# Kernel optimization log

Measured on AMD Instinct MI355X. Metric: run time of the kernel, lower is better.

Reference implementation:

```python
import jax, jax.numpy as jnp
import numpy as np

IN_D = 4096
OUT_D = 4096
NNZ = 1677722
BATCH = 4096
NEG_SLOPE = 0.1


def setup_inputs() -> dict:
    key = jax.random.key(0)
    k_x, k_w, k_b, k_r, k_c = jax.random.split(key, 5)
    x = jax.random.normal(k_x, (BATCH, IN_D), dtype=jnp.float32)
    weight = jax.random.normal(k_w, (NNZ,), dtype=jnp.float32)
    bias = jax.random.normal(k_b, (OUT_D,), dtype=jnp.float32)
    rows = jax.random.randint(k_r, (NNZ,), 0, IN_D, dtype=jnp.int32)
    cols = jax.random.randint(k_c, (NNZ,), 0, OUT_D, dtype=jnp.int32)
    return {"x": x, "weight": weight, "bias": bias, "rows": rows, "cols": cols}


def reference(x, weight, bias, rows, cols):
    # Sparse.forward: W = zeros(in_d, out_d); W[loc] = weight; rho(bias + x @ W)
    W = jnp.zeros((IN_D, OUT_D), dtype=x.dtype).at[rows, cols].set(weight)
    return jax.nn.leaky_relu(bias + x @ W, negative_slope=NEG_SLOPE)
```

## Files before the change

### kernel.cpp

```cpp
#include <hip/hip_runtime.h>
#include <stdint.h>

#define IN_D  4096
#define OUT_D 4096
#define BATCH 4096
#define NEG_SLOPE 0.1f
#define NSEG 8
#define SEGCAP 192

typedef __attribute__((ext_vector_type(8))) short short8;
typedef __attribute__((ext_vector_type(4))) float f32x4;

__device__ __forceinline__ unsigned short f2bf(float f) {
    unsigned u = __builtin_bit_cast(unsigned, f);
    u += 0x7FFFu + ((u >> 16) & 1u);
    return (unsigned short)(u >> 16);
}

__device__ __forceinline__ void gload_lds16(const unsigned short* gsrc, unsigned short* ldsp) {
    __builtin_amdgcn_global_load_lds(
        (const __attribute__((address_space(1))) unsigned int*)gsrc,
        (__attribute__((address_space(3))) unsigned int*)ldsp,
        16, 0, 0);
}

__global__ void zerocnt_kernel(uint4* __restrict__ cnt4) {
    int i = blockIdx.x * blockDim.x + threadIdx.x;
    cnt4[i] = make_uint4(0u, 0u, 0u, 0u);
}

__global__ void bucketcvt_kernel(const int* __restrict__ rows, const int* __restrict__ cols,
                                 const float* __restrict__ w,
                                 unsigned* __restrict__ cnt, uint2* __restrict__ bucket,
                                 int nnz,
                                 const float4* __restrict__ x, ushort4* __restrict__ xb,
                                 int nx4) {
    const int stride = gridDim.x * blockDim.x;
    const int i0 = blockIdx.x * blockDim.x + threadIdx.x;
    const int g = blockIdx.x & (NSEG - 1);
    for (int i = i0; i < nnz; i += stride) {
        int c = cols[i];
        unsigned pos = atomicAdd(&cnt[g * OUT_D + c], 1u);
        if (pos < SEGCAP)
            bucket[((size_t)g * OUT_D + c) * SEGCAP + pos] =
                make_uint2((unsigned)rows[i] | ((unsigned)f2bf(w[i]) << 16),
                           (unsigned)(i + 1));
    }
    for (int i = i0; i < nx4; i += stride) {
        float4 v = x[i];
        ushort4 o;
        o.x = f2bf(v.x); o.y = f2bf(v.y); o.z = f2bf(v.z); o.w = f2bf(v.w);
        xb[i] = o;
    }
}

__global__ __launch_bounds__(256) void coldedup_kernel(
        const uint2* __restrict__ bucket, const unsigned* __restrict__ cnt,
        unsigned short* __restrict__ Wt) {
    __shared__ unsigned long long tag[IN_D];
    const int col = blockIdx.x;
    const int tid = threadIdx.x;

    uint4* t4 = (uint4*)tag;
    #pragma unroll
    for (int j = 0; j < 8; ++j) t4[tid + j * 256] = make_uint4(0u, 0u, 0u, 0u);
    __syncthreads();

    #pragma unroll
    for (int g = 0; g < NSEG; ++g) {
        const int n = min((int)cnt[g * OUT_D + col], SEGCAP);
        const uint2* bk = bucket + ((size_t)g * OUT_D + col) * SEGCAP;
        for (int e = tid; e < n; e += 256) {
            uint2 u = bk[e];
            unsigned long long v = ((unsigned long long)u.y << 16) | (u.x >> 16);
            atomicMax(&tag[u.x & 0xFFFu], v);
        }
    }
    __syncthreads();

    const int r0 = tid * 16;
    short8 o0, o1;
    #pragma unroll
    for (int j = 0; j < 8; ++j) {
        o0[j] = (short)(unsigned short)(tag[r0 + j] & 0xFFFFu);
        o1[j] = (short)(unsigned short)(tag[r0 + 8 + j] & 0xFFFFu);
    }
    *(short8*)&Wt[(size_t)col * IN_D + r0]     = o0;
    *(short8*)&Wt[(size_t)col * IN_D + r0 + 8] = o1;
}

#define BM 256
#define BN 256
#define BK 64
#define NT (IN_D / BK)

#define QUAD(MI0, NI0, BREG) \
    _Pragma("unroll") \
    for (int mi = 0; mi < 4; ++mi) { \
      _Pragma("unroll") \
      for (int ni = 0; ni < 2; ++ni) { \
        _Pragma("unroll") \
        for (int ks = 0; ks < 2; ++ks) { \
          acc[(MI0)+mi][(NI0)+ni] = __builtin_amdgcn_mfma_f32_16x16x32_bf16( \
              a[mi][ks], BREG[ni][ks], acc[(MI0)+mi][(NI0)+ni], 0, 0, 0); \
        } } }

#define PHASE_TAIL(QUADCALL) \
    __builtin_amdgcn_s_barrier(); \
    asm volatile("s_waitcnt lgkmcnt(0)" ::: "memory"); \
    __builtin_amdgcn_sched_barrier(0); \
    __builtin_amdgcn_s_setprio(1); \
    QUADCALL; \
    __builtin_amdgcn_s_setprio(0); \
    __builtin_amdgcn_s_barrier();

#define PREFETCH(D) \
    _Pragma("unroll") \
    for (int mi = 0; mi < 4; ++mi) { \
        a[mi][0] = *(const short8*)&lds[D][0][0][(jA_base + mi * 16) * 64 + kp0]; \
        a[mi][1] = *(const short8*)&lds[D][0][0][(jA_base + mi * 16) * 64 + kp1]; \
    } \
    b0[0][0] = *(const short8*)&lds[D][1][0][jB[0] * 64 + kp0]; \
    b0[0][1] = *(const short8*)&lds[D][1][0][jB[0] * 64 + kp1]; \
    b0[1][0] = *(const short8*)&lds[D][1][0][jB[1] * 64 + kp0]; \
    b0[1][1] = *(const short8*)&lds[D][1][0][jB[1] * 64 + kp1];

__global__ __launch_bounds__(512) void gemm_kernel(
        const unsigned short* __restrict__ Xb,
        const unsigned short* __restrict__ Wt,
        const float* __restrict__ bias,
        float* __restrict__ out)
{
    __shared__ unsigned short lds[2][2][2][128 * 64];

    const int tid  = threadIdx.x;
    const int lane = tid & 63;
    const int wave = tid >> 6;

    const int lin = blockIdx.y * 16 + blockIdx.x;
    const int swz = (lin & 7) * 32 + (lin >> 3);
    const int m0 = (swz >> 4) * BM;
    const int n0 = (swz & 15) * BN;

    const int wm = (wave >> 2) * 128;
    const int wn = (wave & 3) * 64;

    const int lr = lane & 15;
    const int kg = lane >> 4;
    const int x7 = lr & 7;
    const int l8 = lane >> 3;
    const int c8 = lane & 7;

    const int kp0 = ((0 * 4 + kg) ^ x7) * 8;
    const int kp1 = ((1 * 4 + kg) ^ x7) * 8;

    const int jA_base = (wave >> 2) * 64 + lr;
    int jB[4];
    #pragma unroll
    for (int ni = 0; ni < 4; ++ni) {
        int r16 = wn + ni * 16;
        jB[ni] = (r16 & 31) + ((r16 >> 6) << 5) + lr;
    }

    auto stageA = [&](int d, int h, int kt) {
        #pragma unroll
        for (int s = 0; s < 2; ++s) {
            int j = wave * 16 + s * 8 + l8;
            int trow = (j & 63) + h * 64 + ((j >> 6) << 7);
            const unsigned short* src =
                Xb + (size_t)(m0 + trow) * IN_D + kt * BK + 8 * (c8 ^ l8);
            gload_lds16(src, &lds[d][0][h][(wave * 16 + s * 8) * 64]);
        }
    };
    auto stageB = [&](int d, int h, int kt) {
        #pragma unroll
        for (int s = 0; s < 2; ++s) {
            int j = wave * 16 + s * 8 + l8;
            int trow = (j & 31) + h * 32 + ((j >> 5) << 6);
            const unsigned short* src =
                Wt + (size_t)(n0 + trow) * IN_D + kt * BK + 8 * (c8 ^ l8);
            gload_lds16(src, &lds[d][1][h][(wave * 16 + s * 8) * 64]);
        }
    };

    f32x4 acc[8][4] = {};
    short8 a[4][2], b0[2][2], b1[2][2];

    stageA(0, 0, 0); stageB(0, 0, 0); stageB(0, 1, 0); stageA(0, 1, 0);
    stageA(1, 0, 1); stageB(1, 1, 1); stageA(1, 1, 1); stageB(1, 0, 1);
    asm volatile("s_waitcnt vmcnt(8)" ::: "memory");
    __builtin_amdgcn_s_barrier();
    PREFETCH(0)
    asm volatile("s_waitcnt lgkmcnt(0)" ::: "memory");
    __builtin_amdgcn_sched_barrier(0);
    __builtin_amdgcn_s_setprio(1);
    QUAD(0, 0, b0)
    __builtin_amdgcn_s_setprio(0);
    __builtin_amdgcn_s_barrier();

    for (int t = 0; t < NT - 1; ++t) {
        const int cur = t & 1, nxt = cur ^ 1;
        const int kt2 = (t + 2) & (NT - 1);

        b1[0][0] = *(const short8*)&lds[cur][1][1][jB[2] * 64 + kp0];
        b1[0][1] = *(const short8*)&lds[cur][1][1][jB[2] * 64 + kp1];
        b1[1][0] = *(const short8*)&lds[cur][1][1][jB[3] * 64 + kp0];
        b1[1][1] = *(const short8*)&lds[cur][1][1][jB[3] * 64 + kp1];
        stageA(cur, 0, kt2);
        PHASE_TAIL(QUAD(0, 2, b1))

        #pragma unroll
        for (int mi = 0; mi < 4; ++mi) {
            a[mi][0] = *(const short8*)&lds[cur][0][1][(jA_base + mi * 16) * 64 + kp0];
            a[mi][1] = *(const short8*)&lds[cur][0][1][(jA_base + mi * 16) * 64 + kp1];
        }
        stageB(cur, 1, kt2);
        PHASE_TAIL(QUAD(4, 2, b1))

        stageA(cur, 1, kt2);
        asm volatile("s_waitcnt vmcnt(6)" ::: "memory");
        __builtin_amdgcn_s_barrier();
        asm volatile("s_waitcnt lgkmcnt(0)" ::: "memory");
        __builtin_amdgcn_sched_barrier(0);
        __builtin_amdgcn_s_setprio(1);
        QUAD(4, 0, b0)
        __builtin_amdgcn_s_setprio(0);
        PREFETCH(nxt)
        stageB(cur, 0, kt2);
        asm volatile("s_waitcnt lgkmcnt(0)" ::: "memory");
        __builtin_amdgcn_sched_barrier(0);
        __builtin_amdgcn_s_setprio(1);
        QUAD(0, 0, b0)
        __builtin_amdgcn_s_setprio(0);
        __builtin_amdgcn_s_barrier();
    }

    {
        const int cur = (NT - 1) & 1;
        b1[0][0] = *(const short8*)&lds[cur][1][1][jB[2] * 64 + kp0];
        b1[0][1] = *(const short8*)&lds[cur][1][1][jB[2] * 64 + kp1];
        b1[1][0] = *(const short8*)&lds[cur][1][1][jB[3] * 64 + kp0];
        b1[1][1] = *(const short8*)&lds[cur][1][1][jB[3] * 64 + kp1];
        PHASE_TAIL(QUAD(0, 2, b1))
        #pragma unroll
        for (int mi = 0; mi < 4; ++mi) {
            a[mi][0] = *(const short8*)&lds[cur][0][1][(jA_base + mi * 16) * 64 + kp0];
            a[mi][1] = *(const short8*)&lds[cur][0][1][(jA_base + mi * 16) * 64 + kp1];
        }
        asm volatile("s_waitcnt lgkmcnt(0)" ::: "memory");
        __builtin_amdgcn_sched_barrier(0);
        __builtin_amdgcn_s_setprio(1);
        QUAD(4, 2, b1)
        QUAD(4, 0, b0)
        __builtin_amdgcn_s_setprio(0);
    }

    float bfrag[4];
    #pragma unroll
    for (int ni = 0; ni < 4; ++ni) bfrag[ni] = bias[n0 + wn + ni * 16 + lr];

    #pragma unroll
    for (int mi = 0; mi < 8; ++mi) {
        #pragma unroll
        for (int ni = 0; ni < 4; ++ni) {
            const int col = n0 + wn + ni * 16 + lr;
            #pragma unroll
            for (int r = 0; r < 4; ++r) {
                const int row = m0 + wm + mi * 16 + kg * 4 + r;
                float v = acc[mi][ni][r] + bfrag[ni];
                v = v > 0.0f ? v : v * NEG_SLOPE;
                out[(size_t)row * OUT_D + col] = v;
            }
        }
    }
}

extern "C" void kernel_launch(void* const* d_in, const int* in_sizes, int n_in,
                              void* d_out, int out_size, void* d_ws, size_t ws_size,
                              hipStream_t stream) {
    const float* x    = (const float*)d_in[0];
    const float* w    = (const float*)d_in[1];
    const float* bias = (const float*)d_in[2];
    const int*   rows = (const int*)d_in[3];
    const int*   cols = (const int*)d_in[4];
    const int nnz = in_sizes[1];
    float* out = (float*)d_out;

    const size_t NW = (size_t)IN_D * OUT_D;
    unsigned*        cnt    = (unsigned*)d_ws;
    uint2*           bucket = (uint2*)((char*)d_ws + (1u << 20));
    unsigned short*  Wt     = (unsigned short*)((char*)d_ws + (1u << 20)
                                  + (size_t)NSEG * OUT_D * SEGCAP * 8);
    unsigned short*  Xb     = (unsigned short*)((char*)Wt + NW * 2);

    zerocnt_kernel<<<32, 256, 0, stream>>>((uint4*)cnt);
    bucketcvt_kernel<<<2048, 256, 0, stream>>>(rows, cols, w, cnt, bucket, nnz,
                                               (const float4*)x, (ushort4*)Xb,
                                               (int)((size_t)BATCH * IN_D / 4));
    coldedup_kernel<<<OUT_D, 256, 0, stream>>>(bucket, cnt, Wt);

    dim3 grid(OUT_D / BN, BATCH / BM);
    gemm_kernel<<<grid, 512, 0, stream>>>(Xb, Wt, bias, out);
}
```

Before: 204.8 us.

## Restructure GEMM main loop into two barrier phases and widen bucket segments

The GEMM k-loop drops from four compute phases per tile to two. The first half-tile of A/B fragments, including b1, is prefetched at the end of each iteration, and the global-to-LDS staging is regrouped to cut the barriers per iteration. Separately, the bucket scatter grows from 8 to 16 segments with a smaller per-segment capacity, and the counter-zeroing grid doubles to match, aiming to reduce atomic contention when building the dense weight. The new schedule changes vmcnt waits and LDS reuse timing, which risks overwriting buffers still being read or exposing more load latency. The smaller segment capacity may overflow on denser columns.

```diff
diff --git a/kernel.cpp b/kernel.cpp
--- a/kernel.cpp
+++ b/kernel.cpp
@@ -5,8 +5,8 @@
 #define OUT_D 4096
 #define BATCH 4096
 #define NEG_SLOPE 0.1f
-#define NSEG 8
-#define SEGCAP 192
+#define NSEG 16
+#define SEGCAP 120
 
 typedef __attribute__((ext_vector_type(8))) short short8;
 typedef __attribute__((ext_vector_type(4))) float f32x4;
@@ -105,16 +105,7 @@
               a[mi][ks], BREG[ni][ks], acc[(MI0)+mi][(NI0)+ni], 0, 0, 0); \
         } } }
 
-#define PHASE_TAIL(QUADCALL) \
-    __builtin_amdgcn_s_barrier(); \
-    asm volatile("s_waitcnt lgkmcnt(0)" ::: "memory"); \
-    __builtin_amdgcn_sched_barrier(0); \
-    __builtin_amdgcn_s_setprio(1); \
-    QUADCALL; \
-    __builtin_amdgcn_s_setprio(0); \
-    __builtin_amdgcn_s_barrier();
-
-#define PREFETCH(D) \
+#define PREFETCH3(D) \
     _Pragma("unroll") \
     for (int mi = 0; mi < 4; ++mi) { \
         a[mi][0] = *(const short8*)&lds[D][0][0][(jA_base + mi * 16) * 64 + kp0]; \
@@ -123,7 +114,11 @@
     b0[0][0] = *(const short8*)&lds[D][1][0][jB[0] * 64 + kp0]; \
     b0[0][1] = *(const short8*)&lds[D][1][0][jB[0] * 64 + kp1]; \
     b0[1][0] = *(const short8*)&lds[D][1][0][jB[1] * 64 + kp0]; \
-    b0[1][1] = *(const short8*)&lds[D][1][0][jB[1] * 64 + kp1];
+    b0[1][1] = *(const short8*)&lds[D][1][0][jB[1] * 64 + kp1]; \
+    b1[0][0] = *(const short8*)&lds[D][1][1][jB[2] * 64 + kp0]; \
+    b1[0][1] = *(const short8*)&lds[D][1][1][jB[2] * 64 + kp1]; \
+    b1[1][0] = *(const short8*)&lds[D][1][1][jB[3] * 64 + kp0]; \
+    b1[1][1] = *(const short8*)&lds[D][1][1][jB[3] * 64 + kp1];
 
 __global__ __launch_bounds__(512) void gemm_kernel(
         const unsigned short* __restrict__ Xb,
@@ -187,61 +182,53 @@
     short8 a[4][2], b0[2][2], b1[2][2];
 
     stageA(0, 0, 0); stageB(0, 0, 0); stageB(0, 1, 0); stageA(0, 1, 0);
-    stageA(1, 0, 1); stageB(1, 1, 1); stageA(1, 1, 1); stageB(1, 0, 1);
+    stageA(1, 0, 1); stageB(1, 0, 1); stageB(1, 1, 1); stageA(1, 1, 1);
     asm volatile("s_waitcnt vmcnt(8)" ::: "memory");
     __builtin_amdgcn_s_barrier();
-    PREFETCH(0)
-    asm volatile("s_waitcnt lgkmcnt(0)" ::: "memory");
-    __builtin_amdgcn_sched_barrier(0);
-    __builtin_amdgcn_s_setprio(1);
-    QUAD(0, 0, b0)
-    __builtin_amdgcn_s_setprio(0);
-    __builtin_amdgcn_s_barrier();
+    PREFETCH3(0)
 
     for (int t = 0; t < NT - 1; ++t) {
         const int cur = t & 1, nxt = cur ^ 1;
         const int kt2 = (t + 2) & (NT - 1);
 
-        b1[0][0] = *(const short8*)&lds[cur][1][1][jB[2] * 64 + kp0];
-        b1[0][1] = *(const short8*)&lds[cur][1][1][jB[2] * 64 + kp1];
-        b1[1][0] = *(const short8*)&lds[cur][1][1][jB[3] * 64 + kp0];
-        b1[1][1] = *(const short8*)&lds[cur][1][1][jB[3] * 64 + kp1];
+        asm volatile("s_waitcnt lgkmcnt(0)" ::: "memory");
+        __builtin_amdgcn_sched_barrier(0);
+        __builtin_amdgcn_s_setprio(1);
+        QUAD(0, 0, b0)
+        QUAD(0, 2, b1)
+        __builtin_amdgcn_s_setprio(0);
+        __builtin_amdgcn_s_barrier();
+
         stageA(cur, 0, kt2);
-        PHASE_TAIL(QUAD(0, 2, b1))
-
+        stageB(cur, 1, kt2);
+        stageB(cur, 0, kt2);
         #pragma unroll
         for (int mi = 0; mi < 4; ++mi) {
             a[mi][0] = *(const short8*)&lds[cur][0][1][(jA_base + mi * 16) * 64 + kp0];
             a[mi][1] = *(const short8*)&lds[cur][0][1][(jA_base + mi * 16) * 64 + kp1];
         }
-        stageB(cur, 1, kt2);
-        PHASE_TAIL(QUAD(4, 2, b1))
+        asm volatile("s_waitcnt lgkmcnt(0)" ::: "memory");
+        __builtin_amdgcn_sched_barrier(0);
+        __builtin_amdgcn_s_barrier();
 
         stageA(cur, 1, kt2);
-        asm volatile("s_waitcnt vmcnt(6)" ::: "memory");
+        __builtin_amdgcn_s_setprio(1);
+        QUAD(4, 2, b1)
+        QUAD(4, 0, b0)
+        __builtin_amdgcn_s_setprio(0);
+        asm volatile("s_waitcnt vmcnt(8)" ::: "memory");
         __builtin_amdgcn_s_barrier();
-        asm volatile("s_waitcnt lgkmcnt(0)" ::: "memory");
-        __builtin_amdgcn_sched_barrier(0);
-        __builtin_amdgcn_s_setprio(1);
-        QUAD(4, 0, b0)
-        __builtin_amdgcn_s_setprio(0);
-        PREFETCH(nxt)
-        stageB(cur, 0, kt2);
-        asm volatile("s_waitcnt lgkmcnt(0)" ::: "memory");
-        __builtin_amdgcn_sched_barrier(0);
-        __builtin_amdgcn_s_setprio(1);
-        QUAD(0, 0, b0)
-        __builtin_amdgcn_s_setprio(0);
-        __builtin_amdgcn_s_barrier();
+        PREFETCH3(nxt)
     }
 
     {
         const int cur = (NT - 1) & 1;
-        b1[0][0] = *(const short8*)&lds[cur][1][1][jB[2] * 64 + kp0];
-        b1[0][1] = *(const short8*)&lds[cur][1][1][jB[2] * 64 + kp1];
-        b1[1][0] = *(const short8*)&lds[cur][1][1][jB[3] * 64 + kp0];
-        b1[1][1] = *(const short8*)&lds[cur][1][1][jB[3] * 64 + kp1];
-        PHASE_TAIL(QUAD(0, 2, b1))
+        asm volatile("s_waitcnt lgkmcnt(0)" ::: "memory");
+        __builtin_amdgcn_sched_barrier(0);
+        __builtin_amdgcn_s_setprio(1);
+        QUAD(0, 0, b0)
+        QUAD(0, 2, b1)
+        __builtin_amdgcn_s_setprio(0);
         #pragma unroll
         for (int mi = 0; mi < 4; ++mi) {
             a[mi][0] = *(const short8*)&lds[cur][0][1][(jA_base + mi * 16) * 64 + kp0];
@@ -293,7 +280,7 @@
                                   + (size_t)NSEG * OUT_D * SEGCAP * 8);
     unsigned short*  Xb     = (unsigned short*)((char*)Wt + NW * 2);
 
-    zerocnt_kernel<<<32, 256, 0, stream>>>((uint4*)cnt);
+    zerocnt_kernel<<<64, 256, 0, stream>>>((uint4*)cnt);
     bucketcvt_kernel<<<2048, 256, 0, stream>>>(rows, cols, w, cnt, bucket, nnz,
                                                (const float4*)x, (ushort4*)Xb,
                                                (int)((size_t)BATCH * IN_D / 4));
```

After: 230.7 us. 12.7% more time.
